# Optimization experiments

Measured on AMD Instinct MI355X. Metric: run time of the kernel, lower is better.

Reference implementation:

```python
import jax, jax.numpy as jnp
import numpy as np

EMBED_DIM = 1024
N_HEADS = 16
HEAD_DIM = EMBED_DIM // N_HEADS


def setup_inputs() -> dict:
    key = jax.random.key(0)
    k_x, k_wi, k_bi, k_wo, k_bo = jax.random.split(key, 5)
    B, N, C = 4, 2048, EMBED_DIM
    scale = 1.0 / np.sqrt(C)
    return {
        "x": jax.random.normal(k_x, (B, N, C), dtype=jnp.float32),
        "w_in": jax.random.normal(k_wi, (C, 3 * C), dtype=jnp.float32) * scale,
        "b_in": jax.random.normal(k_bi, (3 * C,), dtype=jnp.float32) * 0.01,
        "w_out": jax.random.normal(k_wo, (C, C), dtype=jnp.float32) * scale,
        "b_out": jax.random.normal(k_bo, (C,), dtype=jnp.float32) * 0.01,
    }


def reference(x, w_in, b_in, w_out, b_out):
    B, N, C = x.shape
    H, D = N_HEADS, HEAD_DIM
    qkv = x @ w_in + b_in  # (B, N, 3C)
    q, k, v = jnp.split(qkv, 3, axis=-1)
    # (B, H, N, D)
    q = q.reshape(B, N, H, D).transpose(0, 2, 1, 3)
    k = k.reshape(B, N, H, D).transpose(0, 2, 1, 3)
    v = v.reshape(B, N, H, D).transpose(0, 2, 1, 3)
    # Naive attention: full (B,H,N,N) scores, NO sqrt(d) scaling (as in source)
    scores = jnp.einsum("bhnd,bhmd->bhnm", q, k)
    attn = jax.nn.softmax(scores, axis=-1)
    out = jnp.einsum("bhnm,bhmd->bhnd", attn, v)
    out = out.transpose(0, 2, 1, 3).reshape(B, N, C)
    return out @ w_out + b_out
```

## Files before the change

### kernel.cpp

```cpp
#include <hip/hip_runtime.h>
#include <hip/hip_bf16.h>
#include <stdint.h>

typedef __attribute__((ext_vector_type(8))) __bf16 bf8v;
typedef __attribute__((ext_vector_type(4))) float f4v;

#define L2E 1.44269504088896f

__device__ __forceinline__ unsigned short f2bf(float f) {
  union { float f; unsigned u; } v; v.f = f;
  unsigned r = v.u + 0x7fffu + ((v.u >> 16) & 1u);
  return (unsigned short)(r >> 16);
}

__device__ __forceinline__ unsigned pk2bf(float f0, float f1) {
  union { __hip_bfloat162 h; unsigned u; } c;
  c.h = __float22bfloat162_rn(make_float2(f0, f1));
  return c.u;
}

__device__ __forceinline__ float exp2_hw(float x) {
  return __builtin_amdgcn_exp2f(x);
}

__device__ __forceinline__ void gl_lds16(const void* g, void* l) {
  __builtin_amdgcn_global_load_lds(
      (__attribute__((address_space(1))) void*)(g),
      (__attribute__((address_space(3))) void*)(l), 16, 0, 0);
}

__global__ void prep_kernel(const float* __restrict__ x,
                            const float* __restrict__ w_in,
                            const float* __restrict__ w_out,
                            unsigned short* __restrict__ xb,
                            unsigned short* __restrict__ wiT,
                            unsigned short* __restrict__ woT) {
  __shared__ float tile[32][33];
  int bx = blockIdx.x;
  if (bx < 8192) {
    int i = bx * 256 + threadIdx.x;
    float4 v = ((const float4*)x)[i];
    ushort4 o;
    o.x = f2bf(v.x); o.y = f2bf(v.y); o.z = f2bf(v.z); o.w = f2bf(v.w);
    ((ushort4*)xb)[i] = o;
    return;
  }
  int idx = bx - 8192;
  int bxx = idx & 127, byy = idx >> 7;
  const float* in; unsigned short* out; int C, c0;
  if (bxx < 96) { in = w_in;  out = wiT; C = 3072; c0 = bxx * 32; }
  else          { in = w_out; out = woT; C = 1024; c0 = (bxx - 96) * 32; }
  int r0 = byy * 32;
  int tx = threadIdx.x & 31, ty = threadIdx.x >> 5;
#pragma unroll
  for (int j = 0; j < 4; ++j)
    tile[ty + 8 * j][tx] = in[(size_t)(r0 + ty + 8 * j) * C + c0 + tx];
  __syncthreads();
#pragma unroll
  for (int j = 0; j < 4; ++j)
    out[(size_t)(c0 + ty + 8 * j) * 1024 + r0 + tx] = f2bf(tile[tx][ty + 8 * j]);
}

__global__ __launch_bounds__(512, 2) void gemm1_8ph(
    const unsigned short* __restrict__ A,
    const unsigned short* __restrict__ BT,
    const float* __restrict__ bias,
    unsigned short* __restrict__ qk,
    unsigned short* __restrict__ vtg,
    int K, int nbx, float scale) {
  __shared__ __align__(16) unsigned short As[2][256 * 64];
  __shared__ __align__(16) unsigned short Bs[2][256 * 64];
  const int tid = threadIdx.x;
  const int wave = tid >> 6, lane = tid & 63;
  const int lo = lane & 15, hi = lane >> 4;
  const int wm = wave >> 2, wn = wave & 3;

  const int cpx = gridDim.x >> 3;
  const int s = (blockIdx.x & 7) * cpx + (blockIdx.x >> 3);
  const int by = s / nbx, bx = s - by * nbx;
  const int m0 = by * 256, n0 = bx * 256;

  const int srow = lane >> 3;
  const int scol = (((lane & 7) ^ (srow & 7)) * 8);
  const unsigned short* gA = A + (size_t)(m0 + wave * 8 + srow) * K + scol;
  const unsigned short* gB = BT + (size_t)(n0 + wave * 8 + srow) * K + scol;

  const int csw0 = ((hi ^ (lo & 7)) * 8);
  const int csw1 = (((4 + hi) ^ (lo & 7)) * 8);
  const int rA = wm * 128;
  const int rB = wn * 64;

  f4v acc[8][4] = {};
  const int nt = K >> 6;

  auto stageA = [&](int t, int buf, int half) {
    const unsigned short* g = gA + (size_t)(half * 128) * K + t * 64;
#pragma unroll
    for (int j = 0; j < 2; ++j)
      gl_lds16(g + (size_t)(j * 64) * K, &As[buf][(half * 128 + j * 64 + wave * 8) * 64]);
  };
  auto stageB = [&](int t, int buf, int half) {
    const unsigned short* g = gB + (size_t)(half * 128) * K + t * 64;
#pragma unroll
    for (int j = 0; j < 2; ++j)
      gl_lds16(g + (size_t)(j * 64) * K, &Bs[buf][(half * 128 + j * 64 + wave * 8) * 64]);
  };

  stageA(0, 0, 0); stageA(0, 0, 1);
  stageB(0, 0, 0); stageB(0, 0, 1);
  if (nt > 1) { stageB(1, 1, 0); stageB(1, 1, 1); }
  asm volatile("s_waitcnt vmcnt(4)" ::: "memory");
  __builtin_amdgcn_sched_barrier(0);
  __builtin_amdgcn_s_barrier();

  for (int t = 0; t < nt; ++t) {
    const int c = t & 1;
    bf8v b[4][2];
#pragma unroll
    for (int p = 0; p < 4; ++p) {
      if (p == 0) {
#pragma unroll
        for (int fn = 0; fn < 4; ++fn) {
          b[fn][0] = *(const bf8v*)&Bs[c][(rB + fn * 16 + lo) * 64 + csw0];
          b[fn][1] = *(const bf8v*)&Bs[c][(rB + fn * 16 + lo) * 64 + csw1];
        }
      }
      bf8v a[2][2];
#pragma unroll
      for (int i = 0; i < 2; ++i) {
        a[i][0] = *(const bf8v*)&As[c][(rA + (p * 2 + i) * 16 + lo) * 64 + csw0];
        a[i][1] = *(const bf8v*)&As[c][(rA + (p * 2 + i) * 16 + lo) * 64 + csw1];
      }
      if (p < 2) {
        if (t + 1 < nt) stageA(t + 1, c ^ 1, p);
      } else {
        if (t + 2 < nt) stageB(t + 2, c, p - 2);
      }
      if (p == 3 && t + 1 < nt) {
        if (t + 2 < nt) asm volatile("s_waitcnt vmcnt(4)" ::: "memory");
        else            asm volatile("s_waitcnt vmcnt(0)" ::: "memory");
        __builtin_amdgcn_sched_barrier(0);
      }
      __builtin_amdgcn_s_barrier();
      __builtin_amdgcn_s_setprio(1);
#pragma unroll
      for (int ks = 0; ks < 2; ++ks)
#pragma unroll
        for (int i = 0; i < 2; ++i)
#pragma unroll
          for (int fn = 0; fn < 4; ++fn)
            acc[p * 2 + i][fn] = __builtin_amdgcn_mfma_f32_16x16x32_bf16(
                a[i][ks], b[fn][ks], acc[p * 2 + i][fn], 0, 0, 0);
      __builtin_amdgcn_s_setprio(0);
      __builtin_amdgcn_s_barrier();
    }
  }

#pragma unroll
  for (int i = 0; i < 8; ++i) {
#pragma unroll
    for (int j = 0; j < 4; ++j) {
      const int col = n0 + wn * 64 + j * 16 + lo;
      const int row0 = m0 + wm * 128 + i * 16 + hi * 4;
      const float bb = bias[col];
      if (col < 2048) {
        const float sc = (col < 1024) ? scale : 1.0f;
#pragma unroll
        for (int r = 0; r < 4; ++r)
          qk[(size_t)(row0 + r) * 2048 + col] = f2bf((acc[i][j][r] + bb) * sc);
      } else {
        const int d = (col - 2048) & 63, hh = (col - 2048) >> 6;
        const int bbt = row0 >> 11, tok = row0 & 2047;
        ushort4 o;
        o.x = f2bf(acc[i][j][0] + bb);
        o.y = f2bf(acc[i][j][1] + bb);
        o.z = f2bf(acc[i][j][2] + bb);
        o.w = f2bf(acc[i][j][3] + bb);
        *(ushort4*)&vtg[((((size_t)bbt * 16 + hh) * 64 + d) * 2048) + tok] = o;
      }
    }
  }
}

__global__ __launch_bounds__(512, 2) void gemm2k(
    const unsigned short* __restrict__ A,
    const unsigned short* __restrict__ BT,
    const float* __restrict__ bias,
    float* __restrict__ C,
    int N, int K, int nbx) {
  __shared__ __align__(16) unsigned short As[2][256 * 64];
  __shared__ __align__(16) unsigned short Bs[2][128 * 64];
  const int tid = threadIdx.x;
  const int wave = tid >> 6, lane = tid & 63;
  const int lo = lane & 15, hi = lane >> 4;
  const int wm = wave >> 1, wn = wave & 1;

  const int cpx = gridDim.x >> 3;
  const int s = (blockIdx.x & 7) * cpx + (blockIdx.x >> 3);
  const int by = s / nbx, bx = s - by * nbx;
  const int m0 = by * 256, n0 = bx * 128;

  const int srow = lane >> 3;
  const int scol = (((lane & 7) ^ (srow & 7)) * 8);
  const unsigned short* gA = A + (size_t)(m0 + wave * 8 + srow) * K + scol;
  const unsigned short* gB = BT + (size_t)(n0 + wave * 8 + srow) * K + scol;

  const int csw0 = ((hi ^ (lo & 7)) * 8);
  const int csw1 = (((4 + hi) ^ (lo & 7)) * 8);
  const int rA = wm * 64;
  const int rB = wn * 64;

  f4v acc[4][4] = {};
  const int nt = K >> 6;

#pragma unroll
  for (int j = 0; j < 4; ++j)
    gl_lds16(gA + (size_t)(j * 64) * K, &As[0][(j * 64 + wave * 8) * 64]);
#pragma unroll
  for (int j = 0; j < 2; ++j)
    gl_lds16(gB + (size_t)(j * 64) * K, &Bs[0][(j * 64 + wave * 8) * 64]);

  for (int t = 0; t < nt; ++t) {
    const int c = t & 1;
    __builtin_amdgcn_s_barrier();
    __builtin_amdgcn_sched_barrier(0);
    if (t + 1 < nt) {
      const unsigned short* gA1 = gA + (size_t)(t + 1) * 64;
      const unsigned short* gB1 = gB + (size_t)(t + 1) * 64;
#pragma unroll
      for (int j = 0; j < 4; ++j)
        gl_lds16(gA1 + (size_t)(j * 64) * K, &As[c ^ 1][(j * 64 + wave * 8) * 64]);
#pragma unroll
      for (int j = 0; j < 2; ++j)
        gl_lds16(gB1 + (size_t)(j * 64) * K, &Bs[c ^ 1][(j * 64 + wave * 8) * 64]);
      asm volatile("s_waitcnt vmcnt(6)" ::: "memory");
    } else {
      asm volatile("s_waitcnt vmcnt(0)" ::: "memory");
    }
    __builtin_amdgcn_sched_barrier(0);
    __builtin_amdgcn_s_barrier();
    __builtin_amdgcn_sched_barrier(0);

    bf8v b[4][2];
#pragma unroll
    for (int fn = 0; fn < 4; ++fn) {
      b[fn][0] = *(const bf8v*)&Bs[c][(rB + fn * 16 + lo) * 64 + csw0];
      b[fn][1] = *(const bf8v*)&Bs[c][(rB + fn * 16 + lo) * 64 + csw1];
    }
#pragma unroll
    for (int p = 0; p < 2; ++p) {
      bf8v a[2][2];
#pragma unroll
      for (int i = 0; i < 2; ++i) {
        a[i][0] = *(const bf8v*)&As[c][(rA + (p * 2 + i) * 16 + lo) * 64 + csw0];
        a[i][1] = *(const bf8v*)&As[c][(rA + (p * 2 + i) * 16 + lo) * 64 + csw1];
      }
      __builtin_amdgcn_s_setprio(1);
#pragma unroll
      for (int ks = 0; ks < 2; ++ks)
#pragma unroll
        for (int i = 0; i < 2; ++i)
#pragma unroll
          for (int fn = 0; fn < 4; ++fn)
            acc[p * 2 + i][fn] = __builtin_amdgcn_mfma_f32_16x16x32_bf16(
                a[i][ks], b[fn][ks], acc[p * 2 + i][fn], 0, 0, 0);
      __builtin_amdgcn_s_setprio(0);
    }
  }

#pragma unroll
  for (int i = 0; i < 4; ++i) {
#pragma unroll
    for (int r = 0; r < 4; ++r) {
      int row = m0 + wm * 64 + i * 16 + hi * 4 + r;
#pragma unroll
      for (int j = 0; j < 4; ++j) {
        int col = n0 + wn * 64 + j * 16 + lo;
        C[(size_t)row * N + col] = acc[i][j][r] + bias[col];
      }
    }
  }
}

#define FSTR 72

__global__ __launch_bounds__(256, 2) void flash_attn(
    const unsigned short* __restrict__ qk,
    const unsigned short* __restrict__ vtg,
    unsigned short* __restrict__ y) {
  __shared__ __align__(16) unsigned short Ps[256 * FSTR];
  __shared__ __align__(16) unsigned short Kt[2][64 * FSTR];
  __shared__ __align__(16) unsigned short Vt[2][64 * FSTR];
  const int tid = threadIdx.x;
  const int wave = tid >> 6, lane = tid & 63;
  const int lo = lane & 15, hi = lane >> 4;

  const int lin = blockIdx.x;
  const int swz = (lin & 7) * 64 + (lin >> 3);
  const int q0 = (swz & 7) << 8;
  const int h  = (swz >> 3) & 15;
  const int b  = swz >> 7;

  const size_t base = (size_t)b * 2048 * 2048;
  const int qoff = h * 64, koff = 1024 + h * 64;
  const unsigned short* vsrc = vtg + (size_t)(b * 16 + h) * 64 * 2048;

  const int m_st = tid >> 3, c_st = tid & 7;
  const unsigned short* kg = qk + base + koff;
  float4 rk0, rk1, rv0, rv1;
  auto kv_load = [&](int kt) {
    const int mb = kt * 64;
    rk0 = *(const float4*)(kg + (size_t)(mb + m_st) * 2048 + c_st * 8);
    rk1 = *(const float4*)(kg + (size_t)(mb + m_st + 32) * 2048 + c_st * 8);
    rv0 = *(const float4*)(vsrc + (size_t)m_st * 2048 + mb + c_st * 8);
    rv1 = *(const float4*)(vsrc + (size_t)(m_st + 32) * 2048 + mb + c_st * 8);
  };
  auto kv_write = [&](int buf) {
    *(float4*)&Kt[buf][m_st * FSTR + c_st * 8] = rk0;
    *(float4*)&Kt[buf][(m_st + 32) * FSTR + c_st * 8] = rk1;
    *(float4*)&Vt[buf][m_st * FSTR + c_st * 8] = rv0;
    *(float4*)&Vt[buf][(m_st + 32) * FSTR + c_st * 8] = rv1;
  };

  kv_load(0);

#pragma unroll
  for (int i = 0; i < 8; ++i) {
    int cid = i * 256 + tid;
    int m = cid >> 3, c = cid & 7;
    *(float4*)&Ps[m * FSTR + c * 8] =
        *(const float4*)(qk + base + (size_t)(q0 + m) * 2048 + qoff + c * 8);
  }
  __syncthreads();
  bf8v bq[4][2];
#pragma unroll
  for (int qt = 0; qt < 4; ++qt)
#pragma unroll
    for (int ks = 0; ks < 2; ++ks)
      bq[qt][ks] = *(const bf8v*)&Ps[(wave * 64 + qt * 16 + lo) * FSTR + ks * 32 + hi * 8];

  f4v O[4][4] = {};
  f4v acc_l[4] = {};
  union { bf8v v; unsigned short u[8]; } onesu;
#pragma unroll
  for (int i = 0; i < 8; ++i) onesu.u[i] = 0x3F80;
  const bf8v ones = onesu.v;

  kv_write(0);
  kv_load(1);
  asm volatile("s_waitcnt lgkmcnt(0)" ::: "memory");
  __builtin_amdgcn_s_barrier();
  asm volatile("" ::: "memory");

  for (int kt = 0; kt < 32; ++kt) {
    const int c = kt & 1;
    if (kt < 31) {
      kv_write(c ^ 1);
      if (kt < 30) kv_load(kt + 2);
    }

#pragma unroll
    for (int ct = 0; ct < 4; ++ct) {
      f4v s[4] = {{}, {}, {}, {}};
      __builtin_amdgcn_s_setprio(1);
#pragma unroll
      for (int ks = 0; ks < 2; ++ks) {
        bf8v ak = *(const bf8v*)&Kt[c][(ct * 16 + lo) * FSTR + ks * 32 + hi * 8];
#pragma unroll
        for (int qt = 0; qt < 4; ++qt)
          s[qt] = __builtin_amdgcn_mfma_f32_16x16x32_bf16(ak, bq[qt][ks], s[qt], 0, 0, 0);
      }
      __builtin_amdgcn_s_setprio(0);
#pragma unroll
      for (int qt = 0; qt < 4; ++qt) {
        float p0 = exp2_hw(s[qt][0]), p1 = exp2_hw(s[qt][1]);
        float p2 = exp2_hw(s[qt][2]), p3 = exp2_hw(s[qt][3]);
        uint2 w; w.x = pk2bf(p0, p1); w.y = pk2bf(p2, p3);
        *(uint2*)&Ps[(wave * 64 + qt * 16 + lo) * FSTR + ct * 16 + hi * 4] = w;
      }
    }

#pragma unroll
    for (int ks = 0; ks < 2; ++ks) {
      bf8v ap[4];
#pragma unroll
      for (int qt = 0; qt < 4; ++qt)
        ap[qt] = *(const bf8v*)&Ps[(wave * 64 + qt * 16 + lo) * FSTR + ks * 32 + hi * 8];
      __builtin_amdgcn_s_setprio(1);
#pragma unroll
      for (int qt = 0; qt < 4; ++qt)
        acc_l[qt] = __builtin_amdgcn_mfma_f32_16x16x32_bf16(ap[qt], ones, acc_l[qt], 0, 0, 0);
#pragma unroll
      for (int dt = 0; dt < 4; ++dt) {
        bf8v bv = *(const bf8v*)&Vt[c][(dt * 16 + lo) * FSTR + ks * 32 + hi * 8];
#pragma unroll
        for (int qt = 0; qt < 4; ++qt)
          O[qt][dt] = __builtin_amdgcn_mfma_f32_16x16x32_bf16(ap[qt], bv, O[qt][dt], 0, 0, 0);
      }
      __builtin_amdgcn_s_setprio(0);
    }

    asm volatile("s_waitcnt lgkmcnt(0)" ::: "memory");
    __builtin_amdgcn_s_barrier();
    asm volatile("" ::: "memory");
  }

#pragma unroll
  for (int qt = 0; qt < 4; ++qt) {
#pragma unroll
    for (int r = 0; r < 4; ++r) {
      float inv = 1.f / acc_l[qt][r];
      int row = q0 + wave * 64 + qt * 16 + hi * 4 + r;
      size_t orow = ((size_t)b * 2048 + row) * 1024 + h * 64;
#pragma unroll
      for (int dt = 0; dt < 4; ++dt)
        y[orow + dt * 16 + lo] = f2bf(O[qt][dt][r] * inv);
    }
  }
}

extern "C" void kernel_launch(void* const* d_in, const int* in_sizes, int n_in,
                              void* d_out, int out_size, void* d_ws, size_t ws_size,
                              hipStream_t stream) {
  (void)in_sizes; (void)n_in; (void)out_size; (void)ws_size;
  const float* x     = (const float*)d_in[0];
  const float* w_in  = (const float*)d_in[1];
  const float* b_in  = (const float*)d_in[2];
  const float* w_out = (const float*)d_in[3];
  const float* b_out = (const float*)d_in[4];

  unsigned short* xb  = (unsigned short*)d_ws;
  unsigned short* wiT = xb  + (size_t)8192 * 1024;
  unsigned short* woT = wiT + (size_t)3072 * 1024;
  unsigned short* qk  = woT + (size_t)1024 * 1024;
  unsigned short* vtg = qk  + (size_t)8192 * 2048;
  unsigned short* yb  = vtg + (size_t)64 * 64 * 2048;

  prep_kernel<<<12288, 256, 0, stream>>>(x, w_in, w_out, xb, wiT, woT);

  gemm1_8ph<<<384, 512, 0, stream>>>(xb, wiT, b_in, qk, vtg, 1024, 12, L2E);
  flash_attn<<<512, 256, 0, stream>>>(qk, vtg, yb);
  gemm2k<<<256, 512, 0, stream>>>(yb, woT, b_out, (float*)d_out, 1024, 1024, 8);
}
```

Measured before the change: 272.8 us.

## Use 32x32 MFMA in attention with register-resident P and LDS-staged V transpose

The flash attention kernel moves from 16x16x32 to 32x32x16 bf16 MFMA tiles. The exponentiated scores are packed into bf16 registers and rearranged with v_permlane32_swap into the A-operand layout, so the P round-trip through shared memory and its buffer are gone. Q is also loaded straight from global memory into registers. Separately, the QKV GEMM epilogue now transposes V tiles through LDS so the transposed V store uses coalesced 16-byte writes instead of scattered 8-byte ones. The added cost is extra barriers in the epilogue and higher register pressure from the larger accumulators.

```diff
diff --git a/kernel.cpp b/kernel.cpp
--- a/kernel.cpp
+++ b/kernel.cpp
@@ -4,6 +4,7 @@
 
 typedef __attribute__((ext_vector_type(8))) __bf16 bf8v;
 typedef __attribute__((ext_vector_type(4))) float f4v;
+typedef __attribute__((ext_vector_type(16))) float f16v;
 
 #define L2E 1.44269504088896f
 
@@ -156,27 +157,50 @@
     }
   }
 
-#pragma unroll
-  for (int i = 0; i < 8; ++i) {
-#pragma unroll
-    for (int j = 0; j < 4; ++j) {
-      const int col = n0 + wn * 64 + j * 16 + lo;
-      const int row0 = m0 + wm * 128 + i * 16 + hi * 4;
-      const float bb = bias[col];
-      if (col < 2048) {
+  if (n0 < 2048) {
+#pragma unroll
+    for (int i = 0; i < 8; ++i) {
+#pragma unroll
+      for (int j = 0; j < 4; ++j) {
+        const int col = n0 + wn * 64 + j * 16 + lo;
+        const int row0 = m0 + wm * 128 + i * 16 + hi * 4;
+        const float bb = bias[col];
         const float sc = (col < 1024) ? scale : 1.0f;
 #pragma unroll
         for (int r = 0; r < 4; ++r)
           qk[(size_t)(row0 + r) * 2048 + col] = f2bf((acc[i][j][r] + bb) * sc);
-      } else {
-        const int d = (col - 2048) & 63, hh = (col - 2048) >> 6;
-        const int bbt = row0 >> 11, tok = row0 & 2047;
-        ushort4 o;
-        o.x = f2bf(acc[i][j][0] + bb);
-        o.y = f2bf(acc[i][j][1] + bb);
-        o.z = f2bf(acc[i][j][2] + bb);
-        o.w = f2bf(acc[i][j][3] + bb);
-        *(ushort4*)&vtg[((((size_t)bbt * 16 + hh) * 64 + d) * 2048) + tok] = o;
+      }
+    }
+  } else {
+    unsigned short* T = &As[0][0];
+    const int hh0 = (n0 - 2048) >> 6;
+    const int bbt = m0 >> 11, tokbase = m0 & 2047;
+#pragma unroll 1
+    for (int g = 0; g < 4; ++g) {
+      __syncthreads();
+      if (wn == g) {
+#pragma unroll
+        for (int i = 0; i < 8; ++i)
+#pragma unroll
+          for (int j = 0; j < 4; ++j) {
+            const int col = j * 16 + lo;
+            const int row0 = wm * 128 + i * 16 + hi * 4;
+            const float bb = bias[n0 + wn * 64 + j * 16 + lo];
+            uint2 w;
+            w.x = pk2bf(acc[i][j][0] + bb, acc[i][j][1] + bb);
+            w.y = pk2bf(acc[i][j][2] + bb, acc[i][j][3] + bb);
+            *(uint2*)&T[col * 264 + row0] = w;
+          }
+      }
+      __syncthreads();
+      {
+        const int d = tid >> 3, tk = (tid & 7) * 32;
+        unsigned short* dst =
+            vtg + ((((size_t)bbt * 16 + hh0 + g) * 64 + d) * 2048) + tokbase + tk;
+        const unsigned short* srcl = &T[d * 264 + tk];
+#pragma unroll
+        for (int q4 = 0; q4 < 4; ++q4)
+          *(uint4*)(dst + q4 * 8) = *(const uint4*)(srcl + q4 * 8);
       }
     }
   }
@@ -288,12 +312,11 @@
     const unsigned short* __restrict__ qk,
     const unsigned short* __restrict__ vtg,
     unsigned short* __restrict__ y) {
-  __shared__ __align__(16) unsigned short Ps[256 * FSTR];
   __shared__ __align__(16) unsigned short Kt[2][64 * FSTR];
   __shared__ __align__(16) unsigned short Vt[2][64 * FSTR];
   const int tid = threadIdx.x;
   const int wave = tid >> 6, lane = tid & 63;
-  const int lo = lane & 15, hi = lane >> 4;
+  const int lq = lane & 31, hf = lane >> 5;
 
   const int lin = blockIdx.x;
   const int swz = (lin & 7) * 64 + (lin >> 3);
@@ -304,9 +327,9 @@
   const size_t base = (size_t)b * 2048 * 2048;
   const int qoff = h * 64, koff = 1024 + h * 64;
   const unsigned short* vsrc = vtg + (size_t)(b * 16 + h) * 64 * 2048;
+  const unsigned short* kg = qk + base + koff;
 
   const int m_st = tid >> 3, c_st = tid & 7;
-  const unsigned short* kg = qk + base + koff;
   float4 rk0, rk1, rv0, rv1;
   auto kv_load = [&](int kt) {
     const int mb = kt * 64;
@@ -324,23 +347,16 @@
 
   kv_load(0);
 
-#pragma unroll
-  for (int i = 0; i < 8; ++i) {
-    int cid = i * 256 + tid;
-    int m = cid >> 3, c = cid & 7;
-    *(float4*)&Ps[m * FSTR + c * 8] =
-        *(const float4*)(qk + base + (size_t)(q0 + m) * 2048 + qoff + c * 8);
-  }
-  __syncthreads();
-  bf8v bq[4][2];
-#pragma unroll
-  for (int qt = 0; qt < 4; ++qt)
-#pragma unroll
-    for (int ks = 0; ks < 2; ++ks)
-      bq[qt][ks] = *(const bf8v*)&Ps[(wave * 64 + qt * 16 + lo) * FSTR + ks * 32 + hi * 8];
-
-  f4v O[4][4] = {};
-  f4v acc_l[4] = {};
+  bf8v bq[2][4];
+#pragma unroll
+  for (int qt = 0; qt < 2; ++qt)
+#pragma unroll
+    for (int ks = 0; ks < 4; ++ks)
+      bq[qt][ks] = *(const bf8v*)(qk + base +
+          (size_t)(q0 + wave * 64 + qt * 32 + lq) * 2048 + qoff + ks * 16 + hf * 8);
+
+  f16v O[2][2] = {};
+  f16v acc_l[2] = {};
   union { bf8v v; unsigned short u[8]; } onesu;
 #pragma unroll
   for (int i = 0; i < 8; ++i) onesu.u[i] = 0x3F80;
@@ -359,43 +375,47 @@
       if (kt < 30) kv_load(kt + 2);
     }
 
-#pragma unroll
-    for (int ct = 0; ct < 4; ++ct) {
-      f4v s[4] = {{}, {}, {}, {}};
+    unsigned pk[2][2][8];
+#pragma unroll
+    for (int ct = 0; ct < 2; ++ct) {
+      f16v s[2] = {};
       __builtin_amdgcn_s_setprio(1);
 #pragma unroll
-      for (int ks = 0; ks < 2; ++ks) {
-        bf8v ak = *(const bf8v*)&Kt[c][(ct * 16 + lo) * FSTR + ks * 32 + hi * 8];
-#pragma unroll
-        for (int qt = 0; qt < 4; ++qt)
-          s[qt] = __builtin_amdgcn_mfma_f32_16x16x32_bf16(ak, bq[qt][ks], s[qt], 0, 0, 0);
+      for (int ks = 0; ks < 4; ++ks) {
+        bf8v ak = *(const bf8v*)&Kt[c][(ct * 32 + lq) * FSTR + ks * 16 + hf * 8];
+        s[0] = __builtin_amdgcn_mfma_f32_32x32x16_bf16(ak, bq[0][ks], s[0], 0, 0, 0);
+        s[1] = __builtin_amdgcn_mfma_f32_32x32x16_bf16(ak, bq[1][ks], s[1], 0, 0, 0);
       }
       __builtin_amdgcn_s_setprio(0);
 #pragma unroll
-      for (int qt = 0; qt < 4; ++qt) {
-        float p0 = exp2_hw(s[qt][0]), p1 = exp2_hw(s[qt][1]);
-        float p2 = exp2_hw(s[qt][2]), p3 = exp2_hw(s[qt][3]);
-        uint2 w; w.x = pk2bf(p0, p1); w.y = pk2bf(p2, p3);
-        *(uint2*)&Ps[(wave * 64 + qt * 16 + lo) * FSTR + ct * 16 + hi * 4] = w;
-      }
-    }
-
-#pragma unroll
-    for (int ks = 0; ks < 2; ++ks) {
-      bf8v ap[4];
-#pragma unroll
-      for (int qt = 0; qt < 4; ++qt)
-        ap[qt] = *(const bf8v*)&Ps[(wave * 64 + qt * 16 + lo) * FSTR + ks * 32 + hi * 8];
+      for (int qt = 0; qt < 2; ++qt)
+#pragma unroll
+        for (int dw = 0; dw < 8; ++dw)
+          pk[ct][qt][dw] = pk2bf(exp2_hw(s[qt][2 * dw]), exp2_hw(s[qt][2 * dw + 1]));
+    }
+
+#pragma unroll
+    for (int g = 0; g < 4; ++g) {
+      const int cg = g >> 1, b0 = (2 * g) & 3, b1 = (2 * g + 1) & 3;
+      bf8v ap[2];
+#pragma unroll
+      for (int qt = 0; qt < 2; ++qt) {
+        unsigned a0 = pk[cg][qt][2 * b0], a1 = pk[cg][qt][2 * b0 + 1];
+        unsigned c0 = pk[cg][qt][2 * b1], c1 = pk[cg][qt][2 * b1 + 1];
+        asm("v_permlane32_swap_b32 %0, %1" : "+v"(a0), "+v"(c0));
+        asm("v_permlane32_swap_b32 %0, %1" : "+v"(a1), "+v"(c1));
+        union { unsigned u[4]; bf8v v; } cc;
+        cc.u[0] = a0; cc.u[1] = a1; cc.u[2] = c0; cc.u[3] = c1;
+        ap[qt] = cc.v;
+      }
       __builtin_amdgcn_s_setprio(1);
-#pragma unroll
-      for (int qt = 0; qt < 4; ++qt)
-        acc_l[qt] = __builtin_amdgcn_mfma_f32_16x16x32_bf16(ap[qt], ones, acc_l[qt], 0, 0, 0);
-#pragma unroll
-      for (int dt = 0; dt < 4; ++dt) {
-        bf8v bv = *(const bf8v*)&Vt[c][(dt * 16 + lo) * FSTR + ks * 32 + hi * 8];
-#pragma unroll
-        for (int qt = 0; qt < 4; ++qt)
-          O[qt][dt] = __builtin_amdgcn_mfma_f32_16x16x32_bf16(ap[qt], bv, O[qt][dt], 0, 0, 0);
+      acc_l[0] = __builtin_amdgcn_mfma_f32_32x32x16_bf16(ap[0], ones, acc_l[0], 0, 0, 0);
+      acc_l[1] = __builtin_amdgcn_mfma_f32_32x32x16_bf16(ap[1], ones, acc_l[1], 0, 0, 0);
+#pragma unroll
+      for (int dt = 0; dt < 2; ++dt) {
+        bf8v bv = *(const bf8v*)&Vt[c][(dt * 32 + lq) * FSTR + g * 16 + hf * 8];
+        O[0][dt] = __builtin_amdgcn_mfma_f32_32x32x16_bf16(ap[0], bv, O[0][dt], 0, 0, 0);
+        O[1][dt] = __builtin_amdgcn_mfma_f32_32x32x16_bf16(ap[1], bv, O[1][dt], 0, 0, 0);
       }
       __builtin_amdgcn_s_setprio(0);
     }
@@ -406,15 +426,15 @@
   }
 
 #pragma unroll
-  for (int qt = 0; qt < 4; ++qt) {
-#pragma unroll
-    for (int r = 0; r < 4; ++r) {
+  for (int qt = 0; qt < 2; ++qt) {
+#pragma unroll
+    for (int r = 0; r < 16; ++r) {
       float inv = 1.f / acc_l[qt][r];
-      int row = q0 + wave * 64 + qt * 16 + hi * 4 + r;
+      int row = q0 + wave * 64 + qt * 32 + (r & 3) + 8 * (r >> 2) + 4 * hf;
       size_t orow = ((size_t)b * 2048 + row) * 1024 + h * 64;
 #pragma unroll
-      for (int dt = 0; dt < 4; ++dt)
-        y[orow + dt * 16 + lo] = f2bf(O[qt][dt][r] * inv);
+      for (int dt = 0; dt < 2; ++dt)
+        y[orow + dt * 32 + lq] = f2bf(O[qt][dt][r] * inv);
     }
   }
 }
```

After: 291.8 us. 1.07x slower.
